# Performance work log

Hardware: AMD Instinct MI355X
Metric: run time of the kernel (lower is better)

Reference implementation:

```python
import jax, jax.numpy as jnp
import numpy as np

N = 10000       # num_nodes
E = 1000        # num_hyperedges
STEPS = 30      # horizon


def setup_inputs() -> dict:
    key = jax.random.key(0)
    k1, k2 = jax.random.split(key, 2)
    infected0 = jax.random.uniform(k1, (N,)) < 0.01
    x = jnp.stack([(~infected0).astype(jnp.float32),
                   infected0.astype(jnp.float32),
                   jnp.zeros((N,), jnp.float32)], axis=1)
    H = (jax.random.uniform(k2, (STEPS - 1, E, N)) < 0.001).astype(jnp.float32)
    beta = jnp.full((N,), 0.01, jnp.float32)
    gamma = jnp.full((N,), 0.038, jnp.float32)
    return {"x": x, "H": H, "beta": beta, "gamma": gamma, "steps": STEPS}


def _simulate(x, H, beta, gamma):
    n = x.shape[0]
    key0 = jax.random.key(42)

    def step(carry, H_t):
        p_prev, s_prev, key = carry
        key, k1, k2 = jax.random.split(key, 3)
        infected = s_prev[:, 1]
        # hypergraph Laplacian step: H_t.T @ (H_t @ infected)
        new_cases = beta * (H_t.T @ (H_t @ infected))
        new_rec = gamma * infected
        p = jnp.stack([p_prev[:, 0] - new_cases,
                       p_prev[:, 1] + new_cases - new_rec,
                       p_prev[:, 2] + new_rec], axis=1)
        p = jnp.clip(p, 0.0, 1.0)
        # per-node stochastic SIR state transitions (vectorized)
        u1 = jax.random.uniform(k1, (n,))
        u2 = jax.random.uniform(k2, (n,))
        was_S = s_prev[:, 0] == 1
        was_I = s_prev[:, 1] == 1
        s_to_I = was_S & (u1 < p[:, 1])
        i_event = was_I & (u1 < p[:, 2])
        i_to_R = i_event & (u2 < 0.5)
        i_to_S = i_event & ~(u2 < 0.5)
        new_S = (was_S & ~s_to_I) | i_to_S
        new_I = s_to_I | (was_I & ~i_event)
        new_R = (~was_S & ~was_I) | i_to_R
        s = jnp.stack([new_S, new_I, new_R], axis=1).astype(x.dtype)
        return (p, s, key), (p, s)

    (_, _, _), (p_seq, s_seq) = jax.lax.scan(step, (x, x, key0), H)
    pathogen = jnp.concatenate([x[None], p_seq], axis=0)    # (steps, N, 3)
    state = jnp.concatenate([x[None], s_seq], axis=0)       # (steps, N, 3)
    return pathogen, state


def reference(x, H, beta, gamma, steps):
    # steps == H.shape[0] + 1 by construction
    return _simulate(x, H, beta, gamma)
```

## Files before the change

### kernel.cpp

```cpp
#include <hip/hip_runtime.h>
#include <stdint.h>

constexpr int NN = 10000;
constexpr int EE = 1000;
constexpr int TT = 30;
constexpr int TS = TT - 1;
constexpr int ROW = NN * 3;
constexpr int S_OFF = TT * ROW;
constexpr int CAP_E = 48;
constexpr int CAP_N = 16;

__host__ __device__ inline void tf2x32(uint32_t k0, uint32_t k1,
                                       uint32_t x0, uint32_t x1,
                                       uint32_t &o0, uint32_t &o1) {
  uint32_t ks2 = k0 ^ k1 ^ 0x1BD11BDAu;
  x0 += k0; x1 += k1;
#define TFR(r) do { x0 += x1; x1 = (x1 << (r)) | (x1 >> (32 - (r))); x1 ^= x0; } while (0)
  TFR(13); TFR(15); TFR(26); TFR(6);
  x0 += k1;  x1 += ks2 + 1u;
  TFR(17); TFR(29); TFR(16); TFR(24);
  x0 += ks2; x1 += k0 + 2u;
  TFR(13); TFR(15); TFR(26); TFR(6);
  x0 += k0;  x1 += k1 + 3u;
  TFR(17); TFR(29); TFR(16); TFR(24);
  x0 += k1;  x1 += ks2 + 4u;
  TFR(13); TFR(15); TFR(26); TFR(6);
  x0 += ks2; x1 += k0 + 5u;
#undef TFR
  o0 = x0; o1 = x1;
}

__device__ inline float bits_to_uniform(uint32_t bits) {
  float f = __uint_as_float((bits >> 9) | 0x3F800000u) - 1.0f;
  return f < 0.f ? 0.f : f;
}

struct StepKeys {
  uint32_t k1a[TS], k1b[TS], k2a[TS], k2b[TS];
};

__global__ void k_init(const float* __restrict__ x, float* __restrict__ out,
                       int* __restrict__ node_cnt, float* __restrict__ inf0) {
  int i = blockIdx.x * blockDim.x + threadIdx.x;
  if (i < ROW) { out[i] = x[i]; out[S_OFF + i] = x[i]; }
  if (i < TS * NN) node_cnt[i] = 0;
  if (i < NN) inf0[i] = x[i * 3 + 1];
}

__global__ void k_rand(float* __restrict__ u1, float* __restrict__ u2, StepKeys keys) {
  int t = blockIdx.y;
  int n = blockIdx.x * blockDim.x + threadIdx.x;
  if (n >= NN) return;
  uint32_t a, b;
  tf2x32(keys.k1a[t], keys.k1b[t], 0u, (uint32_t)n, a, b);
  u1[t * NN + n] = bits_to_uniform(a ^ b);
  tf2x32(keys.k2a[t], keys.k2b[t], 0u, (uint32_t)n, a, b);
  u2[t * NN + n] = bits_to_uniform(a ^ b);
}

__global__ void k_scan(const float* __restrict__ H, int* __restrict__ edge_cnt,
                       uint16_t* __restrict__ edge_nodes, int* __restrict__ node_cnt,
                       uint16_t* __restrict__ node_edges) {
  const int row = blockIdx.x;
  const int t = row / EE;
  const int e = row - t * EE;
  __shared__ int cnt;
  __shared__ uint16_t list[CAP_E];
  if (threadIdx.x == 0) cnt = 0;
  __syncthreads();
  const float4* hrow = reinterpret_cast<const float4*>(H + (size_t)row * NN);
  for (int i = threadIdx.x; i < NN / 4; i += blockDim.x) {
    float4 v = hrow[i];
    int b4 = i * 4;
    if (v.x != 0.f) { int p = atomicAdd(&cnt, 1); if (p < CAP_E) list[p] = (uint16_t)(b4 + 0); }
    if (v.y != 0.f) { int p = atomicAdd(&cnt, 1); if (p < CAP_E) list[p] = (uint16_t)(b4 + 1); }
    if (v.z != 0.f) { int p = atomicAdd(&cnt, 1); if (p < CAP_E) list[p] = (uint16_t)(b4 + 2); }
    if (v.w != 0.f) { int p = atomicAdd(&cnt, 1); if (p < CAP_E) list[p] = (uint16_t)(b4 + 3); }
  }
  __syncthreads();
  int c = cnt < CAP_E ? cnt : CAP_E;
  if (threadIdx.x == 0) edge_cnt[row] = c;
  if ((int)threadIdx.x < c) {
    uint16_t m = list[threadIdx.x];
    edge_nodes[(size_t)row * CAP_E + threadIdx.x] = m;
    int slot = atomicAdd(&node_cnt[t * NN + m], 1);
    if (slot < CAP_N) node_edges[((size_t)t * NN + m) * CAP_N + slot] = (uint16_t)e;
  }
}

__global__ void k_edge(const int* __restrict__ edge_cnt, const uint16_t* __restrict__ edge_nodes,
                       const float* __restrict__ inf, float* __restrict__ e_inf, int t) {
  int e = blockIdx.x * blockDim.x + threadIdx.x;
  if (e >= EE) return;
  int row = t * EE + e;
  int ec = edge_cnt[row];
  const uint16_t* el = edge_nodes + (size_t)row * CAP_E;
  float s = 0.f;
  for (int m = 0; m < ec; ++m) s += inf[el[m]];
  e_inf[e] = s;
}

__global__ void k_node(float* __restrict__ out,
                       const int* __restrict__ node_cnt, const uint16_t* __restrict__ node_edges,
                       const float* __restrict__ e_inf,
                       const float* __restrict__ u1t, const float* __restrict__ u2t,
                       const float* __restrict__ beta, const float* __restrict__ gamma_,
                       float* __restrict__ inf_next, int t) {
  int n = blockIdx.x * blockDim.x + threadIdx.x;
  if (n >= NN) return;
  const float* pp = out + (size_t)t * ROW;
  const float* sp = out + S_OFF + (size_t)t * ROW;
  float* po = out + (size_t)(t + 1) * ROW;
  float* so = out + S_OFF + (size_t)(t + 1) * ROW;

  int nc = node_cnt[t * NN + n]; if (nc > CAP_N) nc = CAP_N;
  const uint16_t* nl = node_edges + ((size_t)t * NN + n) * CAP_N;
  float nv = 0.f;
  for (int k = 0; k < nc; ++k) nv += e_inf[nl[k]];

  float s0 = sp[n * 3 + 0], s1 = sp[n * 3 + 1];
  float pp0 = pp[n * 3 + 0], pp1 = pp[n * 3 + 1], pp2 = pp[n * 3 + 2];
  float new_cases = __fmul_rn(beta[n], nv);
  float new_rec   = __fmul_rn(gamma_[n], s1);
  float p0 = fminf(1.f, fmaxf(0.f, __fsub_rn(pp0, new_cases)));
  float p1 = fminf(1.f, fmaxf(0.f, __fsub_rn(__fadd_rn(pp1, new_cases), new_rec)));
  float p2 = fminf(1.f, fmaxf(0.f, __fadd_rn(pp2, new_rec)));

  float u1 = u1t[n];
  float u2 = u2t[n];
  bool was_S  = (s0 == 1.f);
  bool was_I  = (s1 == 1.f);
  bool s_to_I = was_S && (u1 < p1);
  bool i_event = was_I && (u1 < p2);
  bool u2lt   = (u2 < 0.5f);
  bool i_to_R = i_event && u2lt;
  bool i_to_S = i_event && !u2lt;
  bool new_S = (was_S && !s_to_I) || i_to_S;
  bool new_I = s_to_I || (was_I && !i_event);
  bool new_R = (!was_S && !was_I) || i_to_R;

  po[n * 3 + 0] = p0; po[n * 3 + 1] = p1; po[n * 3 + 2] = p2;
  so[n * 3 + 0] = new_S ? 1.f : 0.f;
  so[n * 3 + 1] = new_I ? 1.f : 0.f;
  so[n * 3 + 2] = new_R ? 1.f : 0.f;
  inf_next[n] = new_I ? 1.f : 0.f;
}

extern "C" void kernel_launch(void* const* d_in, const int* in_sizes, int n_in,
                              void* d_out, int out_size, void* d_ws, size_t ws_size,
                              hipStream_t stream) {
  const float* x      = (const float*)d_in[0];
  const float* H      = (const float*)d_in[1];
  const float* beta   = (const float*)d_in[2];
  const float* gamma_ = (const float*)d_in[3];
  float* out = (float*)d_out;

  StepKeys keys;
  uint32_t key0 = 0u, key1 = 42u;
  for (int t = 0; t < TS; ++t) {
    uint32_t a0, b0, a1, b1, a2, b2;
    tf2x32(key0, key1, 0u, 0u, a0, b0);
    tf2x32(key0, key1, 0u, 1u, a1, b1);
    tf2x32(key0, key1, 0u, 2u, a2, b2);
    keys.k1a[t] = a1; keys.k1b[t] = b1; keys.k2a[t] = a2; keys.k2b[t] = b2;
    key0 = a0; key1 = b0;
  }

  size_t off = 0;
  auto take = [&](size_t bytes) { size_t o = off; off += (bytes + 255) & ~(size_t)255; return o; };
  size_t o_ec = take((size_t)TS * EE * sizeof(int));
  size_t o_en = take((size_t)TS * EE * CAP_E * sizeof(uint16_t));
  size_t o_nc = take((size_t)TS * NN * sizeof(int));
  size_t o_ne = take((size_t)TS * NN * CAP_N * sizeof(uint16_t));
  size_t o_ei = take((size_t)EE * sizeof(float));
  size_t o_if = take((size_t)TT * NN * sizeof(float));
  size_t o_u1 = take((size_t)TS * NN * sizeof(float));
  size_t o_u2 = take((size_t)TS * NN * sizeof(float));

  int*      edge_cnt   = (int*)((char*)d_ws + o_ec);
  uint16_t* edge_nodes = (uint16_t*)((char*)d_ws + o_en);
  int*      node_cnt   = (int*)((char*)d_ws + o_nc);
  uint16_t* node_edges = (uint16_t*)((char*)d_ws + o_ne);
  float*    e_inf      = (float*)((char*)d_ws + o_ei);
  float*    inf        = (float*)((char*)d_ws + o_if);
  float*    u1         = (float*)((char*)d_ws + o_u1);
  float*    u2         = (float*)((char*)d_ws + o_u2);

  k_init<<<(TS * NN + 255) / 256, 256, 0, stream>>>(x, out, node_cnt, inf);
  k_rand<<<dim3((NN + 255) / 256, TS), 256, 0, stream>>>(u1, u2, keys);
  k_scan<<<TS * EE, 256, 0, stream>>>(H, edge_cnt, edge_nodes, node_cnt, node_edges);
  for (int t = 0; t < TS; ++t) {
    k_edge<<<(EE + 255) / 256, 256, 0, stream>>>(edge_cnt, edge_nodes,
                                                 inf + (size_t)t * NN, e_inf, t);
    k_node<<<(NN + 255) / 256, 256, 0, stream>>>(out, node_cnt, node_edges, e_inf,
                                                 u1 + (size_t)t * NN, u2 + (size_t)t * NN,
                                                 beta, gamma_, inf + (size_t)(t + 1) * NN, t);
  }
}
```

Measured before the change: 1.823 ms.

## Fuse per-step edge/node kernels into one persistent single-block simulation kernel

Replaces the 58 per-step kernel launches with a single 1024-thread block that loops over all time steps. State is kept as bytes in shared memory and pathogen values in registers. Edge sums are scattered to nodes with shared-memory atomics, so the per-node incidence lists built with global atomics are no longer needed. Edge node lists are stored transposed so that per-edge reads coalesce. The cost is that the whole time loop runs on one compute unit, and the step's output writes are serialized on that one block.

```diff
diff --git a/kernel.cpp b/kernel.cpp
--- a/kernel.cpp
+++ b/kernel.cpp
@@ -8,7 +8,8 @@
 constexpr int ROW = NN * 3;
 constexpr int S_OFF = TT * ROW;
 constexpr int CAP_E = 48;
-constexpr int CAP_N = 16;
+constexpr int SIMT = 1024;
+constexpr int NPT  = 10;
 
 __host__ __device__ inline void tf2x32(uint32_t k0, uint32_t k1,
                                        uint32_t x0, uint32_t x1,
@@ -35,16 +36,11 @@
   return f < 0.f ? 0.f : f;
 }
 
-struct StepKeys {
-  uint32_t k1a[TS], k1b[TS], k2a[TS], k2b[TS];
-};
+struct StepKeys { uint32_t k1a[TS], k1b[TS], k2a[TS], k2b[TS]; };
 
-__global__ void k_init(const float* __restrict__ x, float* __restrict__ out,
-                       int* __restrict__ node_cnt, float* __restrict__ inf0) {
+__global__ void k_init(const float* __restrict__ x, float* __restrict__ out) {
   int i = blockIdx.x * blockDim.x + threadIdx.x;
   if (i < ROW) { out[i] = x[i]; out[S_OFF + i] = x[i]; }
-  if (i < TS * NN) node_cnt[i] = 0;
-  if (i < NN) inf0[i] = x[i * 3 + 1];
 }
 
 __global__ void k_rand(float* __restrict__ u1, float* __restrict__ u2, StepKeys keys) {
@@ -59,8 +55,7 @@
 }
 
 __global__ void k_scan(const float* __restrict__ H, int* __restrict__ edge_cnt,
-                       uint16_t* __restrict__ edge_nodes, int* __restrict__ node_cnt,
-                       uint16_t* __restrict__ node_edges) {
+                       uint16_t* __restrict__ edge_nodes) {
   const int row = blockIdx.x;
   const int t = row / EE;
   const int e = row - t * EE;
@@ -80,70 +75,85 @@
   __syncthreads();
   int c = cnt < CAP_E ? cnt : CAP_E;
   if (threadIdx.x == 0) edge_cnt[row] = c;
-  if ((int)threadIdx.x < c) {
-    uint16_t m = list[threadIdx.x];
-    edge_nodes[(size_t)row * CAP_E + threadIdx.x] = m;
-    int slot = atomicAdd(&node_cnt[t * NN + m], 1);
-    if (slot < CAP_N) node_edges[((size_t)t * NN + m) * CAP_N + slot] = (uint16_t)e;
-  }
+  if ((int)threadIdx.x < c)
+    edge_nodes[((size_t)t * CAP_E + threadIdx.x) * EE + e] = list[threadIdx.x];
 }
 
-__global__ void k_edge(const int* __restrict__ edge_cnt, const uint16_t* __restrict__ edge_nodes,
-                       const float* __restrict__ inf, float* __restrict__ e_inf, int t) {
-  int e = blockIdx.x * blockDim.x + threadIdx.x;
-  if (e >= EE) return;
-  int row = t * EE + e;
-  int ec = edge_cnt[row];
-  const uint16_t* el = edge_nodes + (size_t)row * CAP_E;
-  float s = 0.f;
-  for (int m = 0; m < ec; ++m) s += inf[el[m]];
-  e_inf[e] = s;
-}
+__global__ __launch_bounds__(SIMT, 4)
+void k_sim(float* __restrict__ out, const float* __restrict__ x,
+           const int* __restrict__ edge_cnt, const uint16_t* __restrict__ edge_nodes,
+           const float* __restrict__ u1, const float* __restrict__ u2,
+           const float* __restrict__ beta, const float* __restrict__ gamma_) {
+  __shared__ uint8_t s_st[NN];
+  __shared__ int nv[NN];
+  const int tid = threadIdx.x;
 
-__global__ void k_node(float* __restrict__ out,
-                       const int* __restrict__ node_cnt, const uint16_t* __restrict__ node_edges,
-                       const float* __restrict__ e_inf,
-                       const float* __restrict__ u1t, const float* __restrict__ u2t,
-                       const float* __restrict__ beta, const float* __restrict__ gamma_,
-                       float* __restrict__ inf_next, int t) {
-  int n = blockIdx.x * blockDim.x + threadIdx.x;
-  if (n >= NN) return;
-  const float* pp = out + (size_t)t * ROW;
-  const float* sp = out + S_OFF + (size_t)t * ROW;
-  float* po = out + (size_t)(t + 1) * ROW;
-  float* so = out + S_OFF + (size_t)(t + 1) * ROW;
+  float p0[NPT], p1[NPT], p2[NPT], bet[NPT], gam[NPT];
+#pragma unroll
+  for (int k = 0; k < NPT; ++k) {
+    int n = tid + k * SIMT;
+    if (n < NN) {
+      float x0 = x[n * 3 + 0], x1 = x[n * 3 + 1], x2 = x[n * 3 + 2];
+      p0[k] = x0; p1[k] = x1; p2[k] = x2;
+      s_st[n] = (x1 == 1.f) ? 1 : ((x0 == 1.f) ? 0 : 2);
+      bet[k] = beta[n]; gam[k] = gamma_[n];
+    }
+  }
+  __syncthreads();
 
-  int nc = node_cnt[t * NN + n]; if (nc > CAP_N) nc = CAP_N;
-  const uint16_t* nl = node_edges + ((size_t)t * NN + n) * CAP_N;
-  float nv = 0.f;
-  for (int k = 0; k < nc; ++k) nv += e_inf[nl[k]];
+  for (int t = 0; t < TS; ++t) {
+#pragma unroll
+    for (int k = 0; k < NPT; ++k) { int n = tid + k * SIMT; if (n < NN) nv[n] = 0; }
+    __syncthreads();
 
-  float s0 = sp[n * 3 + 0], s1 = sp[n * 3 + 1];
-  float pp0 = pp[n * 3 + 0], pp1 = pp[n * 3 + 1], pp2 = pp[n * 3 + 2];
-  float new_cases = __fmul_rn(beta[n], nv);
-  float new_rec   = __fmul_rn(gamma_[n], s1);
-  float p0 = fminf(1.f, fmaxf(0.f, __fsub_rn(pp0, new_cases)));
-  float p1 = fminf(1.f, fmaxf(0.f, __fsub_rn(__fadd_rn(pp1, new_cases), new_rec)));
-  float p2 = fminf(1.f, fmaxf(0.f, __fadd_rn(pp2, new_rec)));
+    if (tid < EE) {
+      int row = t * EE + tid;
+      int ec = edge_cnt[row];
+      const uint16_t* base = edge_nodes + (size_t)t * CAP_E * EE + tid;
+      int s = 0;
+      for (int m = 0; m < ec; ++m) s += (s_st[base[(size_t)m * EE]] == 1) ? 1 : 0;
+      for (int m = 0; m < ec; ++m) atomicAdd(&nv[base[(size_t)m * EE]], s);
+    }
+    __syncthreads();
 
-  float u1 = u1t[n];
-  float u2 = u2t[n];
-  bool was_S  = (s0 == 1.f);
-  bool was_I  = (s1 == 1.f);
-  bool s_to_I = was_S && (u1 < p1);
-  bool i_event = was_I && (u1 < p2);
-  bool u2lt   = (u2 < 0.5f);
-  bool i_to_R = i_event && u2lt;
-  bool i_to_S = i_event && !u2lt;
-  bool new_S = (was_S && !s_to_I) || i_to_S;
-  bool new_I = s_to_I || (was_I && !i_event);
-  bool new_R = (!was_S && !was_I) || i_to_R;
+    float* po = out + (size_t)(t + 1) * ROW;
+    float* so = out + S_OFF + (size_t)(t + 1) * ROW;
+    const float* u1t = u1 + (size_t)t * NN;
+    const float* u2t = u2 + (size_t)t * NN;
+#pragma unroll
+    for (int k = 0; k < NPT; ++k) {
+      int n = tid + k * SIMT;
+      if (n < NN) {
+        int st = s_st[n];
+        float s1 = (st == 1) ? 1.f : 0.f;
+        float new_cases = __fmul_rn(bet[k], (float)nv[n]);
+        float new_rec   = __fmul_rn(gam[k], s1);
+        float q0 = fminf(1.f, fmaxf(0.f, __fsub_rn(p0[k], new_cases)));
+        float q1 = fminf(1.f, fmaxf(0.f, __fsub_rn(__fadd_rn(p1[k], new_cases), new_rec)));
+        float q2 = fminf(1.f, fmaxf(0.f, __fadd_rn(p2[k], new_rec)));
+        p0[k] = q0; p1[k] = q1; p2[k] = q2;
 
-  po[n * 3 + 0] = p0; po[n * 3 + 1] = p1; po[n * 3 + 2] = p2;
-  so[n * 3 + 0] = new_S ? 1.f : 0.f;
-  so[n * 3 + 1] = new_I ? 1.f : 0.f;
-  so[n * 3 + 2] = new_R ? 1.f : 0.f;
-  inf_next[n] = new_I ? 1.f : 0.f;
+        float uu1 = u1t[n], uu2 = u2t[n];
+        bool was_S  = (st == 0);
+        bool was_I  = (st == 1);
+        bool s_to_I = was_S && (uu1 < q1);
+        bool i_event = was_I && (uu1 < q2);
+        bool u2lt   = (uu2 < 0.5f);
+        bool i_to_R = i_event && u2lt;
+        bool i_to_S = i_event && !u2lt;
+        bool new_S = (was_S && !s_to_I) || i_to_S;
+        bool new_I = s_to_I || (was_I && !i_event);
+        bool new_R = (!was_S && !was_I) || i_to_R;
+
+        po[n * 3 + 0] = q0; po[n * 3 + 1] = q1; po[n * 3 + 2] = q2;
+        so[n * 3 + 0] = new_S ? 1.f : 0.f;
+        so[n * 3 + 1] = new_I ? 1.f : 0.f;
+        so[n * 3 + 2] = new_R ? 1.f : 0.f;
+        s_st[n] = new_I ? 1 : (new_S ? 0 : 2);
+      }
+    }
+    __syncthreads();
+  }
 }
 
 extern "C" void kernel_launch(void* const* d_in, const int* in_sizes, int n_in,
@@ -170,30 +180,16 @@
   auto take = [&](size_t bytes) { size_t o = off; off += (bytes + 255) & ~(size_t)255; return o; };
   size_t o_ec = take((size_t)TS * EE * sizeof(int));
   size_t o_en = take((size_t)TS * EE * CAP_E * sizeof(uint16_t));
-  size_t o_nc = take((size_t)TS * NN * sizeof(int));
-  size_t o_ne = take((size_t)TS * NN * CAP_N * sizeof(uint16_t));
-  size_t o_ei = take((size_t)EE * sizeof(float));
-  size_t o_if = take((size_t)TT * NN * sizeof(float));
   size_t o_u1 = take((size_t)TS * NN * sizeof(float));
   size_t o_u2 = take((size_t)TS * NN * sizeof(float));
 
   int*      edge_cnt   = (int*)((char*)d_ws + o_ec);
   uint16_t* edge_nodes = (uint16_t*)((char*)d_ws + o_en);
-  int*      node_cnt   = (int*)((char*)d_ws + o_nc);
-  uint16_t* node_edges = (uint16_t*)((char*)d_ws + o_ne);
-  float*    e_inf      = (float*)((char*)d_ws + o_ei);
-  float*    inf        = (float*)((char*)d_ws + o_if);
   float*    u1         = (float*)((char*)d_ws + o_u1);
   float*    u2         = (float*)((char*)d_ws + o_u2);
 
-  k_init<<<(TS * NN + 255) / 256, 256, 0, stream>>>(x, out, node_cnt, inf);
+  k_init<<<(ROW + 255) / 256, 256, 0, stream>>>(x, out);
   k_rand<<<dim3((NN + 255) / 256, TS), 256, 0, stream>>>(u1, u2, keys);
-  k_scan<<<TS * EE, 256, 0, stream>>>(H, edge_cnt, edge_nodes, node_cnt, node_edges);
-  for (int t = 0; t < TS; ++t) {
-    k_edge<<<(EE + 255) / 256, 256, 0, stream>>>(edge_cnt, edge_nodes,
-                                                 inf + (size_t)t * NN, e_inf, t);
-    k_node<<<(NN + 255) / 256, 256, 0, stream>>>(out, node_cnt, node_edges, e_inf,
-                                                 u1 + (size_t)t * NN, u2 + (size_t)t * NN,
-                                                 beta, gamma_, inf + (size_t)(t + 1) * NN, t);
-  }
+  k_scan<<<TS * EE, 256, 0, stream>>>(H, edge_cnt, edge_nodes);
+  k_sim<<<1, SIMT, 0, stream>>>(out, x, edge_cnt, edge_nodes, u1, u2, beta, gamma_);
 }
```

Measured after the change: 1.798 ms. Within noise of the previous version (-1.4%).
